# Kernel optimization log

Measured on AMD Instinct MI355X. Metric: run time of the kernel, lower is better.

## Reference

```python
import jax, jax.numpy as jnp
import numpy as np

WS = 8            # window size
OWIN = 12         # overlapping window: int(8*0.5)+8
HEADS = 4
DHEAD = 16
INNER = 64        # HEADS*DHEAD
DIM = 48
B, H, W = 4, 192, 192
HN, WN = H // WS, W // WS
NW = HN * WN
NK = NW // 2      # deterministic hard-token keep count (ratio=0.5, E[gumbel rate]=0.5)
SCALE = DHEAD ** -0.5


def conv1x1(x, w, b=None):
    y = jnp.einsum('bchw,oc->bohw', x, w)
    return y if b is None else y + b[:, None, None]


def win_part(x):
    # 'b c (h dh) (w dw) -> b (h w) (dh dw) c'
    b, c, h, w = x.shape
    x = x.reshape(b, c, h // WS, WS, w // WS, WS).transpose(0, 2, 4, 3, 5, 1)
    return x.reshape(b, (h // WS) * (w // WS), WS * WS, c)


def win_unpart(x, h, w):
    b, n, l, c = x.shape
    x = x.reshape(b, h // WS, w // WS, WS, WS, c).transpose(0, 5, 1, 3, 2, 4)
    return x.reshape(b, c, h, w)


def unfold_overlap(x):
    # nn.Unfold(kernel=OWIN, stride=WS, pad=(OWIN-WS)//2) -> (b, NW, OWIN^2, c)
    pad = (OWIN - WS) // 2
    xp = jnp.pad(x, ((0, 0), (0, 0), (pad, pad), (pad, pad)))
    hi = (jnp.arange(HN) * WS)[:, None] + jnp.arange(OWIN)[None]
    wi = (jnp.arange(WN) * WS)[:, None] + jnp.arange(OWIN)[None]
    p = xp[:, :, hi[:, None, :, None], wi[None, :, None, :]]  # (b,c,HN,WN,OWIN,OWIN)
    b, c = x.shape[:2]
    return p.reshape(b, c, NW, OWIN * OWIN).transpose(0, 2, 3, 1)


def rel_to_abs(x):
    b, l, m = x.shape
    r = (m + 1) // 2
    x = jnp.pad(x, ((0, 0), (0, 0), (0, 1)))
    flat = jnp.pad(x.reshape(b, l * (m + 1)), ((0, 0), (0, m - l)))
    return flat.reshape(b, l + 1, m)[:, :l, m - r:]


def relative_logits_1d(q, rel_k):
    b, h, w, d = q.shape
    r = (rel_k.shape[0] + 1) // 2
    logits = jnp.einsum('bxyd,rd->bxyr', q, rel_k)
    logits = rel_to_abs(logits.reshape(b * h, w, -1)).reshape(b, h, w, r)
    return jnp.broadcast_to(logits[:, :, None, :, :], (b, h, r, w, r))


def rel_pos_emb(q, rel_h, rel_w):
    # q: (B_, WS*WS, d) -> (B_, WS*WS, OWIN*OWIN)
    B_, L, d = q.shape
    q4 = q.reshape(B_, WS, WS, d)
    lw = relative_logits_1d(q4, rel_w).transpose(0, 1, 3, 2, 4).reshape(B_, L, -1)
    lh = relative_logits_1d(q4.transpose(0, 2, 1, 3), rel_h).transpose(0, 3, 1, 4, 2).reshape(B_, L, -1)
    return lw + lh


def reference(x, condition_global, wq, bq, wk, bk, wv, bv, w_in, b_in, ln_w, ln_b,
              w_sa, b_sa, w_m1, b_m1, w_m2, b_m2, rel_h, rel_w, w_out, b_out):
    b = x.shape[0]
    qs = conv1x1(x, wq, bq)
    ks = conv1x1(x, wk, bk)
    vs = conv1x1(x, wv, bv)

    # deformable condition: per-window normalized coordinate grid
    lin = jnp.linspace(-1.0, 1.0, WS, dtype=x.dtype)
    gy, gx = jnp.meshgrid(lin, lin, indexing='ij')
    wind = jnp.tile(jnp.stack([gy, gx]), (1, HN, WN))
    cond = jnp.concatenate([vs, condition_global, jnp.broadcast_to(wind, (b, 2, H, W))], axis=1)

    # PredictorLG (inference routing)
    t = conv1x1(cond, w_in, b_in)
    mu = t.mean(1, keepdims=True)
    var = ((t - mu) ** 2).mean(1, keepdims=True)
    t = (t - mu) / jnp.sqrt(var + 1e-6)
    t = t * ln_w[:, None, None] + ln_b[:, None, None]
    t = jax.nn.leaky_relu(t, 0.1)
    sa = jax.nn.sigmoid(jax.lax.conv_general_dilated(
        t, w_sa, (1, 1), ((1, 1), (1, 1)),
        dimension_numbers=('NCHW', 'OIHW', 'NCHW')) + b_sa[:, None, None])
    m = win_part(t.mean(1, keepdims=True)).reshape(b, NW, WS * WS)
    h1 = jax.nn.leaky_relu(m @ w_m1.T + b_m1, 0.1)
    pred = jax.nn.softmax(h1 @ w_m2.T + b_m2, axis=-1)
    score = pred[:, :, 0]
    order = jnp.argsort(-score, axis=1)
    idx1, idx2 = order[:, :NK], order[:, NK:]

    # hard branch: gather -> overlapping window attention with rel-pos bias
    qw = jnp.take_along_axis(win_part(qs), idx1[:, :, None, None], axis=1)       # (b,NK,WS^2,INNER)
    kw = jnp.take_along_axis(unfold_overlap(ks), idx1[:, :, None, None], axis=1)  # (b,NK,OWIN^2,INNER)
    vw = jnp.take_along_axis(unfold_overlap(vs), idx1[:, :, None, None], axis=1)
    qh = qw.reshape(b, NK, WS * WS, HEADS, DHEAD)
    kh = kw.reshape(b, NK, OWIN * OWIN, HEADS, DHEAD)
    vh = vw.reshape(b, NK, OWIN * OWIN, HEADS, DHEAD)
    sim = SCALE * jnp.einsum('bnqhd,bnkhd->bnhqk', qh, kh)
    rp = rel_pos_emb(qh.transpose(0, 1, 3, 2, 4).reshape(b * NK * HEADS, WS * WS, DHEAD), rel_h, rel_w)
    sim = sim + rp.reshape(b, NK, HEADS, WS * WS, OWIN * OWIN)
    attn = jax.nn.softmax(sim, axis=-1)
    hard = jnp.einsum('bnhqk,bnkhd->bnqhd', attn, vh).reshape(b, NK, WS * WS, INNER)

    # easy branch: spatial-attention-gated values
    easy = jnp.take_along_axis(win_part(vs * sa), idx2[:, :, None, None], axis=1)

    # scatter-merge (batch_index_fill)
    bar = jnp.arange(b)[:, None]
    merged = jnp.zeros((b, NW, WS * WS, INNER), x.dtype)
    merged = merged.at[bar, idx1].set(hard).at[bar, idx2].set(easy)
    out = win_unpart(merged, H, W)
    return conv1x1(out, w_out, b_out)


def setup_inputs() -> dict:
    key = jax.random.key(0)
    k = jax.random.split(key, 16)
    rn = lambda kk, s, sc=0.05: jax.random.normal(kk, s, jnp.float32) * sc
    return {
        'x': jax.random.normal(k[0], (B, DIM, H, W), jnp.float32),
        'condition_global': jax.random.normal(k[1], (B, 2, H, W), jnp.float32),
        'wq': rn(k[2], (INNER, DIM)), 'bq': jnp.zeros((INNER,), jnp.float32),
        'wk': rn(k[3], (INNER, DIM)), 'bk': jnp.zeros((INNER,), jnp.float32),
        'wv': rn(k[4], (INNER, DIM)), 'bv': jnp.zeros((INNER,), jnp.float32),
        'w_in': rn(k[5], (17, 68)), 'b_in': jnp.zeros((17,), jnp.float32),
        'ln_w': jnp.ones((17,), jnp.float32), 'ln_b': jnp.zeros((17,), jnp.float32),
        'w_sa': rn(k[6], (1, 17, 3, 3)), 'b_sa': jnp.zeros((1,), jnp.float32),
        'w_m1': rn(k[7], (WS, WS * WS)), 'b_m1': jnp.zeros((WS,), jnp.float32),
        'w_m2': rn(k[8], (2, WS)), 'b_m2': jnp.zeros((2,), jnp.float32),
        'rel_h': rn(k[9], (2 * OWIN - 1, DHEAD), DHEAD ** -0.5),
        'rel_w': rn(k[10], (2 * OWIN - 1, DHEAD), DHEAD ** -0.5),
        'w_out': rn(k[11], (DIM, INNER)), 'b_out': jnp.zeros((DIM,), jnp.float32),
    }
```

## Files before the change

kernel.cpp:

```cpp
#include <hip/hip_runtime.h>
#include <math.h>

#define Hh 192
#define Ww 192
#define HWc 36864
#define Bc 4
#define NWc 576
#define NKc 288
#define WNc 24

typedef _Float16 h2_t __attribute__((ext_vector_type(2)));
typedef _Float16 f16x4 __attribute__((ext_vector_type(4)));
typedef float f32x4 __attribute__((ext_vector_type(4)));
typedef unsigned u32x2 __attribute__((ext_vector_type(2)));
__device__ __forceinline__ h2_t u2h(unsigned u) { return __builtin_bit_cast(h2_t, u); }
__device__ __forceinline__ unsigned h2u(h2_t h) { return __builtin_bit_cast(unsigned, h); }
__device__ __forceinline__ h2_t pkrtz(float a, float b) {
    return __builtin_bit_cast(h2_t, __builtin_amdgcn_cvt_pkrtz(a, b));
}
__device__ __forceinline__ f16x4 pk4(float4 v) {
    u32x2 p = { h2u(pkrtz(v.x, v.y)), h2u(pkrtz(v.z, v.w)) };
    return __builtin_bit_cast(f16x4, p);
}
#define L2E 1.44269504f

__global__ __launch_bounds__(256, 1) void k_qkv(const float* __restrict__ x,
    const float* __restrict__ wq, const float* __restrict__ bq,
    const float* __restrict__ wk, const float* __restrict__ bk,
    const float* __restrict__ wvw, const float* __restrict__ bv,
    _Float16* __restrict__ q, _Float16* __restrict__ k, float* __restrict__ v)
{
    __shared__ float xs[132][52];
    __shared__ __align__(16) unsigned char otile[17408];

    int tid = threadIdx.x;
    int blk = blockIdx.x;
    int b = blk / 288;
    int g0 = (blk % 288) * 128;
    const float* xb = x + (size_t)b * 48 * HWc + g0;

    #pragma unroll
    for (int it = 0; it < 6; ++it) {
        int i = it * 256 + tid;
        int c = i >> 5, p4 = (i & 31) * 4;
        float4 xv = *(const float4*)(xb + (size_t)c * HWc + p4);
        xs[p4 + 0][c] = xv.x; xs[p4 + 1][c] = xv.y;
        xs[p4 + 2][c] = xv.z; xs[p4 + 3][c] = xv.w;
    }

    int ln = tid & 63, wave = tid >> 6;
    int dgrp = ln >> 4;
    __syncthreads();

    size_t pbase = (size_t)b * HWc + g0;

    _Float16* qt = (_Float16*)otile;
    #pragma unroll 1
    for (int sel = 0; sel < 2; ++sel) {
        const float* W  = sel ? wk : wq;
        const float* Bi = sel ? bk : bq;
        _Float16* dst   = sel ? k : q;

        f16x4 A[4][3];
        float4 bf[4];
        #pragma unroll
        for (int ot = 0; ot < 4; ++ot) {
            #pragma unroll
            for (int ks = 0; ks < 3; ++ks)
                A[ot][ks] = pk4(*(const float4*)(W + (ot * 16 + (ln & 15)) * 48 + ks * 16 + dgrp * 4));
            bf[ot] = *(const float4*)(Bi + ot * 16 + dgrp * 4);
        }

        #pragma unroll
        for (int t2 = 0; t2 < 2; ++t2) {
            int px = (wave * 2 + t2) * 16 + (ln & 15);
            f16x4 Bf[3];
            #pragma unroll
            for (int ks = 0; ks < 3; ++ks)
                Bf[ks] = pk4(*(const float4*)&xs[px][ks * 16 + dgrp * 4]);
            #pragma unroll
            for (int ot = 0; ot < 4; ++ot) {
                f32x4 D = { bf[ot].x, bf[ot].y, bf[ot].z, bf[ot].w };
                #pragma unroll
                for (int ks = 0; ks < 3; ++ks)
                    D = __builtin_amdgcn_mfma_f32_16x16x16f16(A[ot][ks], Bf[ks], D, 0, 0, 0);
                u32x2 r2 = { h2u(pkrtz(D[0], D[1])), h2u(pkrtz(D[2], D[3])) };
                *(u32x2*)&qt[px * 68 + ot * 16 + dgrp * 4] = r2;
            }
        }
        __syncthreads();
        #pragma unroll
        for (int it = 0; it < 4; ++it) {
            int i = it * 256 + tid;
            int px = i >> 3, seg = i & 7;
            uint4 val = *(const uint4*)&qt[px * 68 + seg * 8];
            *(uint4*)(dst + (pbase + (size_t)px) * 64 + seg * 8) = val;
        }
        __syncthreads();
    }

    {
        f16x4 Avh[4][3], Avl[4][3];
        #pragma unroll
        for (int ot = 0; ot < 4; ++ot)
            #pragma unroll
            for (int ks = 0; ks < 3; ++ks) {
                float4 w4 = *(const float4*)(wvw + (ot * 16 + (ln & 15)) * 48 + ks * 16 + dgrp * 4);
                f16x4 wh = pk4(w4);
                float4 wr = make_float4(w4.x - (float)wh[0], w4.y - (float)wh[1],
                                        w4.z - (float)wh[2], w4.w - (float)wh[3]);
                Avh[ot][ks] = wh;
                Avl[ot][ks] = pk4(wr);
            }
        float4 bvf[4];
        #pragma unroll
        for (int ot = 0; ot < 4; ++ot) bvf[ot] = *(const float4*)(bv + ot * 16 + dgrp * 4);

        float* vt = (float*)otile;
        #pragma unroll 1
        for (int p = 0; p < 2; ++p) {
            int px = (p * 4 + wave) * 16 + (ln & 15);
            f16x4 Bh[3], Bl[3];
            #pragma unroll
            for (int ks = 0; ks < 3; ++ks) {
                float4 x4 = *(const float4*)&xs[px][ks * 16 + dgrp * 4];
                f16x4 xh = pk4(x4);
                float4 xr = make_float4(x4.x - (float)xh[0], x4.y - (float)xh[1],
                                        x4.z - (float)xh[2], x4.w - (float)xh[3]);
                Bh[ks] = xh;
                Bl[ks] = pk4(xr);
            }
            #pragma unroll
            for (int ot = 0; ot < 4; ++ot) {
                f32x4 D = { bvf[ot].x, bvf[ot].y, bvf[ot].z, bvf[ot].w };
                #pragma unroll
                for (int ks = 0; ks < 3; ++ks) {
                    D = __builtin_amdgcn_mfma_f32_16x16x16f16(Avh[ot][ks], Bh[ks], D, 0, 0, 0);
                    D = __builtin_amdgcn_mfma_f32_16x16x16f16(Avh[ot][ks], Bl[ks], D, 0, 0, 0);
                    D = __builtin_amdgcn_mfma_f32_16x16x16f16(Avl[ot][ks], Bh[ks], D, 0, 0, 0);
                }
                *(f32x4*)&vt[(px - p * 64) * 68 + ot * 16 + dgrp * 4] = D;
            }
            __syncthreads();
            #pragma unroll
            for (int it = 0; it < 4; ++it) {
                int i = it * 256 + tid;
                int px2 = i >> 4, seg = i & 15;
                float4 val = *(const float4*)&vt[px2 * 68 + seg * 4];
                *(float4*)(v + (pbase + (size_t)(p * 64 + px2)) * 64 + seg * 4) = val;
            }
            __syncthreads();
        }
    }
}

__global__ __launch_bounds__(192) void k_condsa(const float* __restrict__ vs,
    const float* __restrict__ cg,
    const float* __restrict__ w_in, const float* __restrict__ b_in,
    const float* __restrict__ ln_w, const float* __restrict__ ln_b,
    const float* __restrict__ w_sa, const float* __restrict__ b_sa,
    float* __restrict__ sa, float* __restrict__ mpix)
{
    __shared__ float tl[3][17][194];

    int px = threadIdx.x;
    int blk = blockIdx.x;
    int b = blk / Hh;
    int y = blk % Hh;
    const float step = 2.0f / 7.0f;
    float gx_in = -1.0f + step * (float)(px & 7);

    #pragma unroll 1
    for (int r = 0; r < 3; ++r) {
        int yy = y - 1 + r;
        if ((unsigned)yy >= 192u) continue;
        size_t prem = (size_t)yy * Ww + px;

        float in[68];
        const float* vp = vs + ((size_t)b * HWc + prem) * 64;
        #pragma unroll
        for (int c = 0; c < 64; c += 4) {
            float4 t4 = *(const float4*)(vp + c);
            in[c] = t4.x; in[c+1] = t4.y; in[c+2] = t4.z; in[c+3] = t4.w;
        }
        in[64] = cg[((size_t)b * 2 + 0) * HWc + prem];
        in[65] = cg[((size_t)b * 2 + 1) * HWc + prem];
        in[66] = -1.0f + step * (float)(yy & 7);
        in[67] = gx_in;

        float tv[17];
        float mu = 0.f;
        #pragma unroll
        for (int o = 0; o < 17; ++o) {
            float a = b_in[o];
            const float* wr = w_in + o * 68;
            #pragma unroll
            for (int c = 0; c < 68; ++c) a = fmaf(in[c], wr[c], a);
            tv[o] = a;
            mu += a;
        }
        mu *= (1.f / 17.f);
        float var = 0.f;
        #pragma unroll
        for (int o = 0; o < 17; ++o) { float d = tv[o] - mu; var = fmaf(d, d, var); }
        var *= (1.f / 17.f);
        float rstd = 1.f / sqrtf(var + 1e-6f);

        float msum = 0.f;
        #pragma unroll
        for (int o = 0; o < 17; ++o) {
            float z = (tv[o] - mu) * rstd * ln_w[o] + ln_b[o];
            z = (z >= 0.f) ? z : 0.1f * z;
            tl[r][o][px] = z;
            msum += z;
        }
        if (r == 1) mpix[(size_t)b * HWc + prem] = msum * (1.f / 17.f);
    }
    __syncthreads();

    float a = b_sa[0];
    #pragma unroll 1
    for (int c = 0; c < 17; ++c) {
        const float* wr = w_sa + c * 9;
        #pragma unroll
        for (int ki = 0; ki < 3; ++ki) {
            int yy = y + ki - 1;
            if ((unsigned)yy >= 192u) continue;
            #pragma unroll
            for (int kj = 0; kj < 3; ++kj) {
                int xc = px + kj - 1;
                if ((unsigned)xc >= 192u) continue;
                a = fmaf(tl[ki][c][xc], wr[ki * 3 + kj], a);
            }
        }
    }
    sa[(size_t)b * HWc + (size_t)y * Ww + px] = 1.f / (1.f + expf(-a));
}

__global__ __launch_bounds__(576) void k_score(const float* __restrict__ mpix,
    const float* __restrict__ w_m1, const float* __restrict__ b_m1,
    const float* __restrict__ w_m2, const float* __restrict__ b_m2,
    int* __restrict__ hardl, int* __restrict__ easyl)
{
    __shared__ float sc[NWc];
    int b = blockIdx.x;
    int w = threadIdx.x;
    {
        int hy = w / WNc, wx = w % WNc;
        const float* mp = mpix + (size_t)b * HWc + (hy * 8) * Ww + wx * 8;
        float m[64];
        #pragma unroll
        for (int l = 0; l < 64; ++l) m[l] = mp[(l >> 3) * Ww + (l & 7)];
        float h1[8];
        #pragma unroll
        for (int j = 0; j < 8; ++j) {
            float a = b_m1[j];
            const float* wr = w_m1 + j * 64;
            #pragma unroll
            for (int l = 0; l < 64; ++l) a = fmaf(m[l], wr[l], a);
            h1[j] = (a >= 0.f) ? a : 0.1f * a;
        }
        float l0 = b_m2[0], l1 = b_m2[1];
        #pragma unroll
        for (int j = 0; j < 8; ++j) {
            l0 = fmaf(h1[j], w_m2[j], l0);
            l1 = fmaf(h1[j], w_m2[8 + j], l1);
        }
        float mx = fmaxf(l0, l1);
        float e0 = expf(l0 - mx), e1 = expf(l1 - mx);
        sc[w] = e0 / (e0 + e1);
    }
    __syncthreads();
    float s = sc[w];
    int cnt = 0;
    for (int w2 = 0; w2 < NWc; ++w2) {
        float s2 = sc[w2];
        cnt += ((s2 > s) || (s2 == s && w2 < w)) ? 1 : 0;
    }
    if (cnt < NKc) hardl[b * NKc + cnt] = w;
    else           easyl[b * NKc + (cnt - NKc)] = w;
}

__global__ __launch_bounds__(256) void k_hard(const _Float16* __restrict__ qs,
    const _Float16* __restrict__ ks, const float* __restrict__ vsb,
    const int* __restrict__ hardl,
    const float* __restrict__ relh, const float* __restrict__ relw,
    const float* __restrict__ w_out, const float* __restrict__ b_out,
    float* __restrict__ out)
{
    __shared__ __align__(16) unsigned char smem[49728];
    unsigned char* Kl  = smem;
    unsigned char* Vt  = smem + 18432;
    unsigned char* Rel = smem + 37376;
    _Float16 (*mldsh)[72] = (_Float16 (*)[72])smem;

    int tid = threadIdx.x;
    int blk = blockIdx.x;
    int b = blk / NKc;
    int n = hardl[blk];
    int hy = n / WNc, wx = n % WNc;
    int y0 = hy * 8, x0 = wx * 8;

    #pragma unroll
    for (int i = 0; i < 9; ++i) {
        int idx = i * 256 + tid;
        int px = idx >> 4, c4 = idx & 15;
        int py = px / 12, pxx = px - py * 12;
        int ky = y0 - 2 + py, kx = x0 - 2 + pxx;
        bool ok = ((unsigned)ky < 192u) && ((unsigned)kx < 192u);
        int kyc = min(max(ky, 0), 191), kxc = min(max(kx, 0), 191);
        size_t poff = ((size_t)(b * HWc) + kyc * Ww + kxc) * 64 + c4 * 4;
        uint2 k2 = *(const uint2*)(ks + poff);
        float4 v4 = *(const float4*)(vsb + poff);
        if (!ok) { k2 = make_uint2(0, 0); v4 = make_float4(0, 0, 0, 0); }
        int hd = c4 >> 2, d0 = (c4 & 3) * 4;
        *(uint2*)(Kl + hd * 4608 + px * 32 + (c4 & 3) * 8) = k2;
        _Float16* vh = (_Float16*)(Vt + hd * 4736);
        vh[(d0 + 0) * 148 + px] = (_Float16)v4.x;
        vh[(d0 + 1) * 148 + px] = (_Float16)v4.y;
        vh[(d0 + 2) * 148 + px] = (_Float16)v4.z;
        vh[(d0 + 3) * 148 + px] = (_Float16)v4.w;
    }
    if (tid < 16) *(unsigned*)(Rel + 12288 + tid * 4) = 0u;

    int h = __builtin_amdgcn_readfirstlane(tid >> 6);
    int l = tid & 63;
    int dgrp = l >> 4;

    {
        int qr = l >> 3, qc = l & 7;
        const _Float16* qp = qs + ((size_t)(b * HWc) + (y0 + qr) * Ww + (x0 + qc)) * 64 + h * 16;
        uint4 q0 = *(const uint4*)qp;
        uint4 q1 = *(const uint4*)(qp + 8);
        h2_t qhp[8] = { u2h(q0.x), u2h(q0.y), u2h(q0.z), u2h(q0.w),
                        u2h(q1.x), u2h(q1.y), u2h(q1.z), u2h(q1.w) };
        float qv[16];
        #pragma unroll
        for (int j = 0; j < 8; ++j) { qv[2*j] = (float)qhp[j].x; qv[2*j+1] = (float)qhp[j].y; }

        float rw[12], rh[12];
        #pragma unroll
        for (int kc = 0; kc < 12; ++kc) {
            const float* rp = relw + (kc - qc + 11) * 16;
            float a = 0.f;
            #pragma unroll
            for (int j = 0; j < 4; ++j) {
                float4 t4 = *(const float4*)(rp + j * 4);
                a = fmaf(qv[j*4+0], t4.x, a); a = fmaf(qv[j*4+1], t4.y, a);
                a = fmaf(qv[j*4+2], t4.z, a); a = fmaf(qv[j*4+3], t4.w, a);
            }
            rw[kc] = a;
        }
        #pragma unroll
        for (int kr = 0; kr < 12; ++kr) {
            const float* rp = relh + (kr - qr + 11) * 16;
            float a = 0.f;
            #pragma unroll
            for (int j = 0; j < 4; ++j) {
                float4 t4 = *(const float4*)(rp + j * 4);
                a = fmaf(qv[j*4+0], t4.x, a); a = fmaf(qv[j*4+1], t4.y, a);
                a = fmaf(qv[j*4+2], t4.z, a); a = fmaf(qv[j*4+3], t4.w, a);
            }
            rh[kr] = a;
        }
        unsigned rr[12];
        #pragma unroll
        for (int j = 0; j < 6; ++j) rr[j]     = h2u(pkrtz(L2E * rw[2*j], L2E * rw[2*j+1]));
        #pragma unroll
        for (int j = 0; j < 6; ++j) rr[6 + j] = h2u(pkrtz(L2E * rh[2*j], L2E * rh[2*j+1]));
        uint4* dst = (uint4*)(Rel + h * 3072 + l * 48);
        dst[0] = make_uint4(rr[0], rr[1], rr[2],  rr[3]);
        dst[1] = make_uint4(rr[4], rr[5], rr[6],  rr[7]);
        dst[2] = make_uint4(rr[8], rr[9], rr[10], rr[11]);
    }
    __syncthreads();

    f16x4 qb[4], rb1[4], rb2[4];
    {
        const h2_t qsc = { (_Float16)(0.25f * L2E), (_Float16)(0.25f * L2E) };
        #pragma unroll
        for (int tn = 0; tn < 4; ++tn) {
            int q = tn * 16 + (l & 15);
            int qr = q >> 3, qc = q & 7;
            uint2 raw = *(const uint2*)(qs + ((size_t)(b * HWc) + (y0 + qr) * Ww + (x0 + qc)) * 64 + h * 16 + dgrp * 4);
            h2_t lo = u2h(raw.x) * qsc, hi = u2h(raw.y) * qsc;
            u32x2 packed = { h2u(lo), h2u(hi) };
            qb[tn] = __builtin_bit_cast(f16x4, packed);
            const unsigned char* rbase = Rel + h * 3072 + q * 48 + dgrp * 8;
            rb1[tn] = *(const f16x4*)rbase;
            rb2[tn] = *(const f16x4*)(rbase + 32);
        }
    }

    f32x4 Oacc[4];
    float lsum[4];
    #pragma unroll
    for (int tn = 0; tn < 4; ++tn) { Oacc[tn] = (f32x4){0.f,0.f,0.f,0.f}; lsum[tn] = 0.f; }
    const f32x4 zf = {0.f, 0.f, 0.f, 0.f};
    const float SH = 3.0f * L2E;

    f16x4 kaA = *(const f16x4*)(Kl + h * 4608 + (l & 15) * 32 + dgrp * 8);
    f16x4 vaA = *(const f16x4*)(Vt + h * 4736 + (l & 15) * 296 + (dgrp * 4) * 2);

    #pragma unroll 1
    for (int tm = 0; tm < 9; ++tm) {
        int tmn = (tm + 1 < 9) ? tm + 1 : 0;
        f16x4 kaB = *(const f16x4*)(Kl + h * 4608 + (tmn * 16 + (l & 15)) * 32 + dgrp * 8);
        f16x4 vaB = *(const f16x4*)(Vt + h * 4736 + (l & 15) * 296 + (tmn * 16 + dgrp * 4) * 2);

        int key = tm * 16 + (l & 15);
        int kr = (key * 2731) >> 15;
        int kc = key - kr * 12;
        f16x4 oh1, oh2;
        #pragma unroll
        for (int i = 0; i < 4; ++i) {
            int a1 = 4 * dgrp + i;
            bool v1 = (a1 < 12) ? (kc == a1) : (kr == a1 - 12);
            oh1[i] = v1 ? (_Float16)1.0f : (_Float16)0.0f;
            int a2 = 16 + 4 * dgrp + i;
            bool v2 = (a2 < 24) && (kr == a2 - 12);
            oh2[i] = v2 ? (_Float16)1.0f : (_Float16)0.0f;
        }

        #pragma unroll
        for (int tn = 0; tn < 4; ++tn) {
            f32x4 s = __builtin_amdgcn_mfma_f32_16x16x16f16(kaA, qb[tn],  zf, 0, 0, 0);
            s       = __builtin_amdgcn_mfma_f32_16x16x16f16(oh1, rb1[tn], s,  0, 0, 0);
            s       = __builtin_amdgcn_mfma_f32_16x16x16f16(oh2, rb2[tn], s,  0, 0, 0);
            float e0 = exp2f(s[0] - SH);
            float e1 = exp2f(s[1] - SH);
            float e2 = exp2f(s[2] - SH);
            float e3 = exp2f(s[3] - SH);
            lsum[tn] += (e0 + e1) + (e2 + e3);
            u32x2 pp = { h2u(pkrtz(e0, e1)), h2u(pkrtz(e2, e3)) };
            f16x4 pb = __builtin_bit_cast(f16x4, pp);
            Oacc[tn] = __builtin_amdgcn_mfma_f32_16x16x16f16(vaA, pb, Oacc[tn], 0, 0, 0);
        }
        kaA = kaB; vaA = vaB;
    }

    __syncthreads();
    #pragma unroll
    for (int tn = 0; tn < 4; ++tn) {
        float s = lsum[tn];
        s += __shfl_xor(s, 16);
        s += __shfl_xor(s, 32);
        float inv = 1.f / s;
        int q = tn * 16 + (l & 15);
        u32x2 w2 = { h2u(pkrtz(Oacc[tn][0] * inv, Oacc[tn][1] * inv)),
                     h2u(pkrtz(Oacc[tn][2] * inv, Oacc[tn][3] * inv)) };
        *(u32x2*)&mldsh[q][h * 16 + dgrp * 4] = w2;
    }
    __syncthreads();

    {
        int tn2 = h;
        int pxl = tn2 * 16 + (l & 15);
        f16x4 bf[4];
        #pragma unroll
        for (int ks = 0; ks < 4; ++ks)
            bf[ks] = *(const f16x4*)&mldsh[pxl][ks * 16 + dgrp * 4];

        int gy = y0 + (pxl >> 3), gx = x0 + (pxl & 7);
        #pragma unroll
        for (int ot = 0; ot < 3; ++ot) {
            float4 bi = *(const float4*)(b_out + ot * 16 + dgrp * 4);
            f32x4 Cacc = { bi.x, bi.y, bi.z, bi.w };
            #pragma unroll
            for (int ks = 0; ks < 4; ++ks) {
                float4 wv = *(const float4*)(w_out + (ot * 16 + (l & 15)) * 64 + ks * 16 + dgrp * 4);
                Cacc = __builtin_amdgcn_mfma_f32_16x16x16f16(pk4(wv), bf[ks], Cacc, 0, 0, 0);
            }
            #pragma unroll
            for (int i = 0; i < 4; ++i)
                out[((size_t)(b * 48 + ot * 16 + dgrp * 4 + i)) * HWc + gy * Ww + gx] = Cacc[i];
        }
    }
}

__global__ __launch_bounds__(256) void k_easy(const float* __restrict__ vsb,
    const float* __restrict__ sab, const int* __restrict__ easyl,
    const float* __restrict__ w_out, const float* __restrict__ b_out,
    float* __restrict__ out)
{
    __shared__ __align__(16) _Float16 mldsh[64][72];

    int tid = threadIdx.x;
    int blk = blockIdx.x;
    int b = blk / NKc;
    int n = easyl[blk];
    int hy = n / WNc, wx = n % WNc;
    int y0 = hy * 8, x0 = wx * 8;

    {
        int l = tid >> 2, part = tid & 3;
        int gy = y0 + (l >> 3), gx = x0 + (l & 7);
        const float* vp = vsb + ((size_t)(b * HWc) + gy * Ww + gx) * 64 + part * 16;
        float sv = sab[(size_t)b * HWc + gy * Ww + gx];
        #pragma unroll
        for (int j = 0; j < 4; ++j) {
            float4 v4 = *(const float4*)(vp + j * 4);
            u32x2 w2 = { h2u(pkrtz(v4.x * sv, v4.y * sv)),
                         h2u(pkrtz(v4.z * sv, v4.w * sv)) };
            *(u32x2*)&mldsh[l][part * 16 + j * 4] = w2;
        }
    }
    __syncthreads();

    {
        int l = tid & 63;
        int tn2 = __builtin_amdgcn_readfirstlane(tid >> 6);
        int dgrp = l >> 4;
        int pxl = tn2 * 16 + (l & 15);
        f16x4 bf[4];
        #pragma unroll
        for (int ks = 0; ks < 4; ++ks)
            bf[ks] = *(const f16x4*)&mldsh[pxl][ks * 16 + dgrp * 4];

        int gy = y0 + (pxl >> 3), gx = x0 + (pxl & 7);
        #pragma unroll
        for (int ot = 0; ot < 3; ++ot) {
            float4 bi = *(const float4*)(b_out + ot * 16 + dgrp * 4);
            f32x4 Cacc = { bi.x, bi.y, bi.z, bi.w };
            #pragma unroll
            for (int ks = 0; ks < 4; ++ks) {
                float4 wv = *(const float4*)(w_out + (ot * 16 + (l & 15)) * 64 + ks * 16 + dgrp * 4);
                Cacc = __builtin_amdgcn_mfma_f32_16x16x16f16(pk4(wv), bf[ks], Cacc, 0, 0, 0);
            }
            #pragma unroll
            for (int i = 0; i < 4; ++i)
                out[((size_t)(b * 48 + ot * 16 + dgrp * 4 + i)) * HWc + gy * Ww + gx] = Cacc[i];
        }
    }
}

extern "C" void kernel_launch(void* const* d_in, const int* in_sizes, int n_in,
                              void* d_out, int out_size, void* d_ws, size_t ws_size,
                              hipStream_t stream)
{
    const float* x    = (const float*)d_in[0];
    const float* cg   = (const float*)d_in[1];
    const float* wq   = (const float*)d_in[2];
    const float* bq   = (const float*)d_in[3];
    const float* wk   = (const float*)d_in[4];
    const float* bk   = (const float*)d_in[5];
    const float* wv   = (const float*)d_in[6];
    const float* bv   = (const float*)d_in[7];
    const float* w_in = (const float*)d_in[8];
    const float* b_in = (const float*)d_in[9];
    const float* ln_w = (const float*)d_in[10];
    const float* ln_b = (const float*)d_in[11];
    const float* w_sa = (const float*)d_in[12];
    const float* b_sa = (const float*)d_in[13];
    const float* w_m1 = (const float*)d_in[14];
    const float* b_m1 = (const float*)d_in[15];
    const float* w_m2 = (const float*)d_in[16];
    const float* b_m2 = (const float*)d_in[17];
    const float* rel_h= (const float*)d_in[18];
    const float* rel_w= (const float*)d_in[19];
    const float* w_out= (const float*)d_in[20];
    const float* b_out= (const float*)d_in[21];
    float* out = (float*)d_out;

    _Float16* qsh = (_Float16*)d_ws;
    _Float16* ksh = qsh + (size_t)Bc * 64 * HWc;
    float* vs   = (float*)(ksh + (size_t)Bc * 64 * HWc);
    float* sa   = vs + (size_t)Bc * 64 * HWc;
    float* mpix = sa + (size_t)Bc * HWc;
    int*   hardl= (int*)(mpix + (size_t)Bc * HWc);
    int*   easyl= hardl + Bc * NKc;

    k_qkv   <<<1152, 256, 0, stream>>>(x, wq, bq, wk, bk, wv, bv, qsh, ksh, vs);
    k_condsa<<<Bc * Hh, 192, 0, stream>>>(vs, cg, w_in, b_in, ln_w, ln_b, w_sa, b_sa, sa, mpix);
    k_score <<<4, 576, 0, stream>>>(mpix, w_m1, b_m1, w_m2, b_m2, hardl, easyl);
    k_easy  <<<1152, 256, 0, stream>>>(vs, sa, easyl, w_out, b_out, out);
    k_hard  <<<1152, 256, 0, stream>>>(qsh, ksh, vs, hardl, rel_h, rel_w, w_out, b_out, out);
}
```

Measured before the change: 175.9 us.

## Merge easy and hard window kernels and pass rel-pos logits via shuffles

Merges the separate easy-window and hard-window kernels into one launch, with block index selecting the path, which removes a kernel launch and its tail gap. The relative-position logits are moved from shared memory to register shuffles, shrinking shared memory from about 49.7KB to 37.4KB, which may allow more resident blocks per CU. The cost is extra shuffle and select instructions per tile, and the easy blocks now reserve the larger hard-path shared allocation.

```diff
diff --git a/kernel.cpp b/kernel.cpp
--- a/kernel.cpp
+++ b/kernel.cpp
@@ -281,21 +281,71 @@
     else           easyl[b * NKc + (cnt - NKc)] = w;
 }
 
-__global__ __launch_bounds__(256) void k_hard(const _Float16* __restrict__ qs,
+__global__ __launch_bounds__(256) void k_win(const _Float16* __restrict__ qs,
     const _Float16* __restrict__ ks, const float* __restrict__ vsb,
-    const int* __restrict__ hardl,
+    const float* __restrict__ sab,
+    const int* __restrict__ hardl, const int* __restrict__ easyl,
     const float* __restrict__ relh, const float* __restrict__ relw,
     const float* __restrict__ w_out, const float* __restrict__ b_out,
     float* __restrict__ out)
 {
-    __shared__ __align__(16) unsigned char smem[49728];
-    unsigned char* Kl  = smem;
-    unsigned char* Vt  = smem + 18432;
-    unsigned char* Rel = smem + 37376;
+    __shared__ __align__(16) unsigned char smem[37376];
+    unsigned char* Kl = smem;
+    unsigned char* Vt = smem + 18432;
     _Float16 (*mldsh)[72] = (_Float16 (*)[72])smem;
 
     int tid = threadIdx.x;
     int blk = blockIdx.x;
+    int l = tid & 63;
+    int dgrp = l >> 4;
+
+    if (blk >= Bc * NKc) {
+        int blk2 = blk - Bc * NKc;
+        int b = blk2 / NKc;
+        int n = easyl[blk2];
+        int hy = n / WNc, wx = n % WNc;
+        int y0 = hy * 8, x0 = wx * 8;
+
+        {
+            int lp = tid >> 2, part = tid & 3;
+            int gy = y0 + (lp >> 3), gx = x0 + (lp & 7);
+            const float* vp = vsb + ((size_t)(b * HWc) + gy * Ww + gx) * 64 + part * 16;
+            float sv = sab[(size_t)b * HWc + gy * Ww + gx];
+            #pragma unroll
+            for (int j = 0; j < 4; ++j) {
+                float4 v4 = *(const float4*)(vp + j * 4);
+                u32x2 w2 = { h2u(pkrtz(v4.x * sv, v4.y * sv)),
+                             h2u(pkrtz(v4.z * sv, v4.w * sv)) };
+                *(u32x2*)&mldsh[lp][part * 16 + j * 4] = w2;
+            }
+        }
+        __syncthreads();
+        {
+            int tn2 = __builtin_amdgcn_readfirstlane(tid >> 6);
+            int pxl = tn2 * 16 + (l & 15);
+            f16x4 bfr[4];
+            #pragma unroll
+            for (int ksi = 0; ksi < 4; ++ksi)
+                bfr[ksi] = *(const f16x4*)&mldsh[pxl][ksi * 16 + dgrp * 4];
+
+            int gy = y0 + (pxl >> 3), gx = x0 + (pxl & 7);
+            #pragma unroll
+            for (int ot = 0; ot < 3; ++ot) {
+                float4 bi = *(const float4*)(b_out + ot * 16 + dgrp * 4);
+                f32x4 Cacc = { bi.x, bi.y, bi.z, bi.w };
+                #pragma unroll
+                for (int ksi = 0; ksi < 4; ++ksi) {
+                    float4 wv = *(const float4*)(w_out + (ot * 16 + (l & 15)) * 64 + ksi * 16 + dgrp * 4);
+                    Cacc = __builtin_amdgcn_mfma_f32_16x16x16f16(pk4(wv), bfr[ksi], Cacc, 0, 0, 0);
+                }
+                #pragma unroll
+                for (int i = 0; i < 4; ++i)
+                    out[((size_t)(b * 48 + ot * 16 + dgrp * 4 + i)) * HWc + gy * Ww + gx] = Cacc[i];
+            }
+        }
+        return;
+    }
+
     int b = blk / NKc;
     int n = hardl[blk];
     int hy = n / WNc, wx = n % WNc;
@@ -321,12 +371,10 @@
         vh[(d0 + 2) * 148 + px] = (_Float16)v4.z;
         vh[(d0 + 3) * 148 + px] = (_Float16)v4.w;
     }
-    if (tid < 16) *(unsigned*)(Rel + 12288 + tid * 4) = 0u;
 
     int h = __builtin_amdgcn_readfirstlane(tid >> 6);
-    int l = tid & 63;
-    int dgrp = l >> 4;
-
+
+    unsigned rr[12];
     {
         int qr = l >> 3, qc = l & 7;
         const _Float16* qp = qs + ((size_t)(b * HWc) + (y0 + qr) * Ww + (x0 + qc)) * 64 + h * 16;
@@ -363,34 +411,38 @@
             }
             rh[kr] = a;
         }
-        unsigned rr[12];
         #pragma unroll
         for (int j = 0; j < 6; ++j) rr[j]     = h2u(pkrtz(L2E * rw[2*j], L2E * rw[2*j+1]));
         #pragma unroll
         for (int j = 0; j < 6; ++j) rr[6 + j] = h2u(pkrtz(L2E * rh[2*j], L2E * rh[2*j+1]));
-        uint4* dst = (uint4*)(Rel + h * 3072 + l * 48);
-        dst[0] = make_uint4(rr[0], rr[1], rr[2],  rr[3]);
-        dst[1] = make_uint4(rr[4], rr[5], rr[6],  rr[7]);
-        dst[2] = make_uint4(rr[8], rr[9], rr[10], rr[11]);
-    }
-    __syncthreads();
+    }
 
     f16x4 qb[4], rb1[4], rb2[4];
     {
         const h2_t qsc = { (_Float16)(0.25f * L2E), (_Float16)(0.25f * L2E) };
         #pragma unroll
         for (int tn = 0; tn < 4; ++tn) {
-            int q = tn * 16 + (l & 15);
-            int qr = q >> 3, qc = q & 7;
+            int qq = tn * 16 + (l & 15);
+            int qr = qq >> 3, qc = qq & 7;
             uint2 raw = *(const uint2*)(qs + ((size_t)(b * HWc) + (y0 + qr) * Ww + (x0 + qc)) * 64 + h * 16 + dgrp * 4);
             h2_t lo = u2h(raw.x) * qsc, hi = u2h(raw.y) * qsc;
             u32x2 packed = { h2u(lo), h2u(hi) };
             qb[tn] = __builtin_bit_cast(f16x4, packed);
-            const unsigned char* rbase = Rel + h * 3072 + q * 48 + dgrp * 8;
-            rb1[tn] = *(const f16x4*)rbase;
-            rb2[tn] = *(const f16x4*)(rbase + 32);
-        }
-    }
+
+            unsigned s[12];
+            #pragma unroll
+            for (int j = 0; j < 12; ++j) s[j] = (unsigned)__shfl((int)rr[j], qq);
+            unsigned a0 = (dgrp == 0) ? s[0] : (dgrp == 1) ? s[2] : (dgrp == 2) ? s[4] : s[6];
+            unsigned a1 = (dgrp == 0) ? s[1] : (dgrp == 1) ? s[3] : (dgrp == 2) ? s[5] : s[7];
+            unsigned b0 = (dgrp == 0) ? s[8] : (dgrp == 1) ? s[10] : 0u;
+            unsigned b1 = (dgrp == 0) ? s[9] : (dgrp == 1) ? s[11] : 0u;
+            u32x2 p1 = { a0, a1 };
+            u32x2 p2 = { b0, b1 };
+            rb1[tn] = __builtin_bit_cast(f16x4, p1);
+            rb2[tn] = __builtin_bit_cast(f16x4, p2);
+        }
+    }
+    __syncthreads();
 
     f32x4 Oacc[4];
     float lsum[4];
@@ -446,20 +498,19 @@
         s += __shfl_xor(s, 16);
         s += __shfl_xor(s, 32);
         float inv = 1.f / s;
-        int q = tn * 16 + (l & 15);
+        int qq = tn * 16 + (l & 15);
         u32x2 w2 = { h2u(pkrtz(Oacc[tn][0] * inv, Oacc[tn][1] * inv)),
                      h2u(pkrtz(Oacc[tn][2] * inv, Oacc[tn][3] * inv)) };
-        *(u32x2*)&mldsh[q][h * 16 + dgrp * 4] = w2;
+        *(u32x2*)&mldsh[qq][h * 16 + dgrp * 4] = w2;
     }
     __syncthreads();
 
     {
-        int tn2 = h;
-        int pxl = tn2 * 16 + (l & 15);
-        f16x4 bf[4];
-        #pragma unroll
-        for (int ks = 0; ks < 4; ++ks)
-            bf[ks] = *(const f16x4*)&mldsh[pxl][ks * 16 + dgrp * 4];
+        int pxl = h * 16 + (l & 15);
+        f16x4 bfr[4];
+        #pragma unroll
+        for (int ksi = 0; ksi < 4; ++ksi)
+            bfr[ksi] = *(const f16x4*)&mldsh[pxl][ksi * 16 + dgrp * 4];
 
         int gy = y0 + (pxl >> 3), gx = x0 + (pxl & 7);
         #pragma unroll
@@ -467,65 +518,9 @@
             float4 bi = *(const float4*)(b_out + ot * 16 + dgrp * 4);
             f32x4 Cacc = { bi.x, bi.y, bi.z, bi.w };
             #pragma unroll
-            for (int ks = 0; ks < 4; ++ks) {
-                float4 wv = *(const float4*)(w_out + (ot * 16 + (l & 15)) * 64 + ks * 16 + dgrp * 4);
-                Cacc = __builtin_amdgcn_mfma_f32_16x16x16f16(pk4(wv), bf[ks], Cacc, 0, 0, 0);
-            }
-            #pragma unroll
-            for (int i = 0; i < 4; ++i)
-                out[((size_t)(b * 48 + ot * 16 + dgrp * 4 + i)) * HWc + gy * Ww + gx] = Cacc[i];
-        }
-    }
-}
-
-__global__ __launch_bounds__(256) void k_easy(const float* __restrict__ vsb,
-    const float* __restrict__ sab, const int* __restrict__ easyl,
-    const float* __restrict__ w_out, const float* __restrict__ b_out,
-    float* __restrict__ out)
-{
-    __shared__ __align__(16) _Float16 mldsh[64][72];
-
-    int tid = threadIdx.x;
-    int blk = blockIdx.x;
-    int b = blk / NKc;
-    int n = easyl[blk];
-    int hy = n / WNc, wx = n % WNc;
-    int y0 = hy * 8, x0 = wx * 8;
-
-    {
-        int l = tid >> 2, part = tid & 3;
-        int gy = y0 + (l >> 3), gx = x0 + (l & 7);
-        const float* vp = vsb + ((size_t)(b * HWc) + gy * Ww + gx) * 64 + part * 16;
-        float sv = sab[(size_t)b * HWc + gy * Ww + gx];
-        #pragma unroll
-        for (int j = 0; j < 4; ++j) {
-            float4 v4 = *(const float4*)(vp + j * 4);
-            u32x2 w2 = { h2u(pkrtz(v4.x * sv, v4.y * sv)),
-                         h2u(pkrtz(v4.z * sv, v4.w * sv)) };
-            *(u32x2*)&mldsh[l][part * 16 + j * 4] = w2;
-        }
-    }
-    __syncthreads();
-
-    {
-        int l = tid & 63;
-        int tn2 = __builtin_amdgcn_readfirstlane(tid >> 6);
-        int dgrp = l >> 4;
-        int pxl = tn2 * 16 + (l & 15);
-        f16x4 bf[4];
-        #pragma unroll
-        for (int ks = 0; ks < 4; ++ks)
-            bf[ks] = *(const f16x4*)&mldsh[pxl][ks * 16 + dgrp * 4];
-
-        int gy = y0 + (pxl >> 3), gx = x0 + (pxl & 7);
-        #pragma unroll
-        for (int ot = 0; ot < 3; ++ot) {
-            float4 bi = *(const float4*)(b_out + ot * 16 + dgrp * 4);
-            f32x4 Cacc = { bi.x, bi.y, bi.z, bi.w };
-            #pragma unroll
-            for (int ks = 0; ks < 4; ++ks) {
-                float4 wv = *(const float4*)(w_out + (ot * 16 + (l & 15)) * 64 + ks * 16 + dgrp * 4);
-                Cacc = __builtin_amdgcn_mfma_f32_16x16x16f16(pk4(wv), bf[ks], Cacc, 0, 0, 0);
+            for (int ksi = 0; ksi < 4; ++ksi) {
+                float4 wv = *(const float4*)(w_out + (ot * 16 + (l & 15)) * 64 + ksi * 16 + dgrp * 4);
+                Cacc = __builtin_amdgcn_mfma_f32_16x16x16f16(pk4(wv), bfr[ksi], Cacc, 0, 0, 0);
             }
             #pragma unroll
             for (int i = 0; i < 4; ++i)
@@ -573,6 +568,6 @@
     k_qkv   <<<1152, 256, 0, stream>>>(x, wq, bq, wk, bk, wv, bv, qsh, ksh, vs);
     k_condsa<<<Bc * Hh, 192, 0, stream>>>(vs, cg, w_in, b_in, ln_w, ln_b, w_sa, b_sa, sa, mpix);
     k_score <<<4, 576, 0, stream>>>(mpix, w_m1, b_m1, w_m2, b_m2, hardl, easyl);
-    k_easy  <<<1152, 256, 0, stream>>>(vs, sa, easyl, w_out, b_out, out);
-    k_hard  <<<1152, 256, 0, stream>>>(qsh, ksh, vs, hardl, rel_h, rel_w, w_out, b_out, out);
-}
+    k_win   <<<2 * Bc * NKc, 256, 0, stream>>>(qsh, ksh, vs, sa, hardl, easyl,
+                                               rel_h, rel_w, w_out, b_out, out);
+}
```

After: 172.4 us (median of 2 runs). 1.02x faster.
